# Kernel tuning notes

Measured on AMD Instinct MI355X. Metric: run time of the kernel, lower is better.

Reference implementation:

```python
import jax, jax.numpy as jnp
import numpy as np

ATTN_DIM = 1024
LATENT_DIM = 1024
N_HEADS = 16
HEAD_SIZE = ATTN_DIM // N_HEADS


def setup_inputs() -> dict:
    key = jax.random.key(0)
    ks = jax.random.split(key, 7)
    B, T = 2, 2048
    s_in = 1.0 / np.sqrt(LATENT_DIM)
    s_a = 1.0 / np.sqrt(ATTN_DIM)
    return {
        "x": jax.random.normal(ks[0], (B, T, LATENT_DIM), jnp.float32),
        "w_attn": jax.random.normal(ks[1], (LATENT_DIM, ATTN_DIM), jnp.float32) * s_in,
        "b_attn": jnp.zeros((ATTN_DIM,), jnp.float32),
        "w_qkv": jax.random.normal(ks[2], (ATTN_DIM, 3 * ATTN_DIM), jnp.float32) * s_a,
        "b_qkv": jnp.zeros((3 * ATTN_DIM,), jnp.float32),
        "w_proj": jax.random.normal(ks[3], (ATTN_DIM, ATTN_DIM), jnp.float32) * s_a,
        "b_proj": jnp.zeros((ATTN_DIM,), jnp.float32),
    }


def reference(x, w_attn, b_attn, w_qkv, b_qkv, w_proj, b_proj):
    # x: [B, T, latent_dim]
    h = jnp.einsum("btl,lc->btc", x, w_attn) + b_attn  # [B,T,C]
    B, T, C = h.shape
    qkv = jnp.einsum("btc,cd->btd", h, w_qkv) + b_qkv  # [B,T,3C]
    q, k, v = jnp.split(qkv, 3, axis=2)
    def heads(t):  # [B,T,C] -> [B,H,T,hs]
        return t.reshape(B, T, N_HEADS, HEAD_SIZE).transpose(0, 2, 1, 3)
    q, k, v = heads(q), heads(k), heads(v)
    scale = 1.0 / np.sqrt(HEAD_SIZE)
    scores = jnp.einsum("bhqd,bhkd->bhqk", q, k) * scale  # [B,H,T,T]
    attn = jax.nn.softmax(scores, axis=-1)
    out = jnp.einsum("bhqk,bhkd->bhqd", attn, v)  # [B,H,T,hs]
    out = out.transpose(0, 2, 1, 3).reshape(B, T, C)
    return jnp.einsum("btc,cd->btd", out, w_proj) + b_proj
```

## Files before the change

kernel.cpp:

```cpp
#include <hip/hip_runtime.h>

typedef unsigned short u16;
typedef unsigned int u32;
typedef __bf16 bf16x8 __attribute__((ext_vector_type(8)));
typedef float f32x4 __attribute__((ext_vector_type(4)));
typedef float f32x16 __attribute__((ext_vector_type(16)));
typedef unsigned uint2v __attribute__((ext_vector_type(2)));

typedef const __attribute__((address_space(1))) void* gcp_t;
typedef __attribute__((address_space(3))) void* lp_t;
#define GLDS16(g, l) __builtin_amdgcn_global_load_lds((gcp_t)(g), (lp_t)(l), 16, 0, 0)

__device__ __forceinline__ u16 f2bf(float f) {
  unsigned int u = __builtin_bit_cast(unsigned int, f);
  u += 0x7fffu + ((u >> 16) & 1u);
  return (u16)(u >> 16);
}
__device__ __forceinline__ u16 bfc(float f) {
  return __builtin_bit_cast(u16, (__bf16)f);
}
__device__ __forceinline__ u32 pkbf(float lo, float hi) {
  return (u32)bfc(lo) | ((u32)bfc(hi) << 16);
}
__device__ __forceinline__ float ex2(float x) {
  return __builtin_amdgcn_exp2f(x);
}

__global__ __launch_bounds__(256) void prep(const float* __restrict__ x, u16* __restrict__ xb,
                                            const float* __restrict__ wa, u16* __restrict__ wTa,
                                            const float* __restrict__ wq, u16* __restrict__ wTq,
                                            const float* __restrict__ wp, u16* __restrict__ wTp) {
  __shared__ float tile[32][33];
  const int idx = (int)blockIdx.x;
  const int tid = (int)threadIdx.x;
  if (idx < 2048) {
    long i = ((long)idx * 256 + tid) * 8;
    float4 a = *(const float4*)(x + i);
    float4 b = *(const float4*)(x + i + 4);
    union { u16 u[8]; int4 v; } pk;
    pk.u[0] = f2bf(a.x); pk.u[1] = f2bf(a.y); pk.u[2] = f2bf(a.z); pk.u[3] = f2bf(a.w);
    pk.u[4] = f2bf(b.x); pk.u[5] = f2bf(b.y); pk.u[6] = f2bf(b.z); pk.u[7] = f2bf(b.w);
    *(int4*)(xb + i) = pk.v;
    return;
  }
  const float* in; u16* out; int K, N, bx, by;
  if (idx < 3072) {
    int id = idx - 2048; in = wa; out = wTa; K = 1024; N = 1024; bx = id & 31; by = id >> 5;
  } else if (idx < 6144) {
    int id = idx - 3072; in = wq; out = wTq; K = 1024; N = 3072; bx = id % 96; by = id / 96;
  } else {
    int id = idx - 6144; in = wp; out = wTp; K = 1024; N = 1024; bx = id & 31; by = id >> 5;
  }
  const int n0 = bx * 32, k0 = by * 32;
  const int tx = tid & 31, ty = tid >> 5;
#pragma unroll
  for (int i = 0; i < 4; ++i)
    tile[ty + i * 8][tx] = in[(long)(k0 + ty + i * 8) * N + n0 + tx];
  __syncthreads();
#pragma unroll
  for (int i = 0; i < 4; ++i)
    out[(long)(n0 + ty + i * 8) * K + k0 + tx] = f2bf(tile[tx][ty + i * 8]);
}

template <int BM, int BN, int WN_WAVES, typename OutT, bool VSPLIT = false>
__global__ __launch_bounds__(256) void gemm_bt(const u16* __restrict__ A,
                                               const u16* __restrict__ Bt,
                                               const float* __restrict__ bias,
                                               OutT* __restrict__ C,
                                               u16* __restrict__ vout,
                                               int M, int N, int K) {
  constexpr int WM = BM / (4 / WN_WAVES);
  constexpr int WN = BN / WN_WAVES;
  constexpr int MF = WM / 16, NF = WN / 16;
  constexpr int STG = 2 * BM * 32 + 2 * BN * 32;
  constexpr int TRN = VSPLIT ? 128 * 136 : 0;
  constexpr int PSZ = STG > TRN ? STG : TRN;
  __shared__ __align__(16) u16 pool[PSZ];
  u16* lA0 = pool;
  u16* lB0 = pool + 2 * BM * 32;
  const int tid = (int)threadIdx.x;
  const int ln = tid & 63;
  const int w = tid >> 6;
  const int wr = w / WN_WAVES, wc = w % WN_WAVES;
  const int lr = ln & 15, lg = ln >> 4;

  const int nwg = (int)(gridDim.x * gridDim.y);
  const int lin = (int)(blockIdx.y * gridDim.x + blockIdx.x);
  const int cpx = nwg >> 3;
  const int swzb = (lin & 7) * cpx + (lin >> 3);
  const int bx = swzb % (int)gridDim.x;
  const int by = swzb / (int)gridDim.x;
  const long mBase = (long)by * BM;
  const long nBase = (long)bx * BN;

  f32x4 acc[MF][NF] = {};

  const int r0 = ln >> 2;
  const int c0 = (ln & 3) * 8;

  auto stage = [&](int buf, int k0) {
#pragma unroll
    for (int i = 0; i < BM / 64; ++i) {
      const int br = (i * 4 + w) * 16;
      GLDS16(A + (mBase + br + r0) * K + k0 + c0, lA0 + buf * BM * 32 + br * 32);
    }
#pragma unroll
    for (int i = 0; i < BN / 64; ++i) {
      const int br = (i * 4 + w) * 16;
      GLDS16(Bt + (nBase + br + r0) * K + k0 + c0, lB0 + buf * BN * 32 + br * 32);
    }
  };

  stage(0, 0);
  __syncthreads();
  int cur = 0;
  for (int k0 = 0; k0 < K; k0 += 32) {
    if (k0 + 32 < K) stage(cur ^ 1, k0 + 32);
    bf16x8 af[MF], bfv[NF];
#pragma unroll
    for (int mi = 0; mi < MF; ++mi)
      af[mi] = *(const bf16x8*)&lA0[cur * BM * 32 + (wr * WM + mi * 16 + lr) * 32 + lg * 8];
#pragma unroll
    for (int ni = 0; ni < NF; ++ni)
      bfv[ni] = *(const bf16x8*)&lB0[cur * BN * 32 + (wc * WN + ni * 16 + lr) * 32 + lg * 8];
#pragma unroll
    for (int mi = 0; mi < MF; ++mi)
#pragma unroll
      for (int ni = 0; ni < NF; ++ni)
        acc[mi][ni] = __builtin_amdgcn_mfma_f32_16x16x32_bf16(af[mi], bfv[ni],
                                                              acc[mi][ni], 0, 0, 0);
    __syncthreads();
    cur ^= 1;
  }

  if (VSPLIT && nBase >= 2048) {
#pragma unroll
    for (int ni = 0; ni < NF; ++ni) {
      const int cl = wc * WN + ni * 16 + lr;
      const float bv = bias[nBase + cl];
#pragma unroll
      for (int mi = 0; mi < MF; ++mi) {
#pragma unroll
        for (int j = 0; j < 4; ++j) {
          const int rl = wr * WM + mi * 16 + lg * 4 + j;
          pool[cl * 136 + rl] = bfc(acc[mi][ni][j] + bv);
        }
      }
    }
    __syncthreads();
    const int c = tid >> 1, half = tid & 1;
    const long cglob = nBase + c - 2048;
    const int hh2 = (int)(cglob >> 6), d = (int)(cglob & 63);
    const int bb = (int)(mBase >> 11);
    const int t0 = (int)(mBase & 2047);
    u16* dst = vout + ((long)(bb * 16 + hh2) * 64 + d) * 2048 + t0 + half * 64;
    const u16* srcp = &pool[c * 136 + half * 64];
#pragma unroll
    for (int i = 0; i < 8; ++i)
      *(int4*)(dst + i * 8) = *(const int4*)(srcp + i * 8);
    return;
  }

#pragma unroll
  for (int ni = 0; ni < NF; ++ni) {
    const long col = nBase + wc * WN + ni * 16 + lr;
    const float bv = bias[col];
#pragma unroll
    for (int mi = 0; mi < MF; ++mi) {
      const long row = mBase + wr * WM + mi * 16 + lg * 4;
#pragma unroll
      for (int j = 0; j < 4; ++j) {
        float v = acc[mi][ni][j] + bv;
        if constexpr (sizeof(OutT) == 2) {
          C[(row + j) * N + col] = (OutT)f2bf(v);
        } else {
          C[(row + j) * N + col] = v;
        }
      }
    }
  }
}

__global__ __launch_bounds__(512, 4) void attn_fwd(const u16* __restrict__ qkv,
                                                   const u16* __restrict__ vt,
                                                   u16* __restrict__ outp) {
  __shared__ __align__(16) u16 smemf[32768];
  const int tid = (int)threadIdx.x;
  const int ln = tid & 63;
  const int l31 = tid & 31;
  const int hiH = (tid >> 5) & 1;
  const int w = tid >> 6;
  const int g = w >> 2;
  const int qw = w & 3;
  const int bid0 = (int)blockIdx.x;
  const int bid = ((bid0 & 7) << 6) | (bid0 >> 3);
  const int qt = bid & 15;
  const int bh = bid >> 4;
  const int b = bh >> 4;
  const int hh = bh & 15;

  const float SCALE = 0.125f * 1.44269504088896f;

  const long qrow = (long)(b * 2048 + qt * 128 + qw * 32 + l31);
  const u16* Qp = qkv + qrow * 3072 + hh * 64;
  bf16x8 qf[4];
#pragma unroll
  for (int ks = 0; ks < 4; ++ks) {
    union { u16 u[8]; int4 i4; bf16x8 v; } in, ov;
    in.i4 = *(const int4*)(Qp + ks * 16 + hiH * 8);
#pragma unroll
    for (int e = 0; e < 8; ++e) {
      float f = __builtin_bit_cast(float, (u32)in.u[e] << 16) * SCALE;
      ov.u[e] = f2bf(f);
    }
    qf[ks] = ov.v;
  }

  f32x16 o[2] = {};
  float mrow = -1e30f, lsum = 0.f;

  const u16* Kbase = qkv + ((long)b * 2048) * 3072 + 1024 + hh * 64;
  const u16* Vbase = vt + (long)bh * 64 * 2048;

  const int sr = ln >> 3;
  const int scm = ln & 7;

  const int sw = (l31 & 7) << 4;
  const char* lds0 = (const char*)smemf + g * 32768 + l31 * 128;
  const char* kbse[4];
#pragma unroll
  for (int ks = 0; ks < 4; ++ks) kbse[ks] = lds0 + ((ks * 32 + hiH * 16) ^ sw);

  auto stageKV = [&](int buf, int t) {
    const int kv0 = (g * 16 + t) * 64;
    u16* dstK = smemf + g * 16384 + buf * 8192;
#pragma unroll
    for (int i = 0; i < 2; ++i) {
      const int br = (i * 4 + qw) * 8;
      const int r = br + sr;
      const int cs = scm ^ (r & 7);
      GLDS16(Kbase + (long)(kv0 + r) * 3072 + cs * 8, dstK + br * 64);
      GLDS16(Vbase + (long)r * 2048 + kv0 + cs * 8, dstK + 4096 + br * 64);
    }
  };

  stageKV(0, 0);
  __syncthreads();

  auto tile = [&](int buf, int kt) {
    if (kt + 1 < 16) stageKV(buf ^ 1, kt + 1);
    const int boff = buf * 16384;

    f32x16 st[2] = {};
#pragma unroll
    for (int t = 0; t < 2; ++t)
#pragma unroll
      for (int ks = 0; ks < 4; ++ks) {
        const bf16x8 kf = *(const bf16x8*)(kbse[ks] + boff + t * 4096);
        st[t] = __builtin_amdgcn_mfma_f32_32x32x16_bf16(kf, qf[ks], st[t], 0, 0, 0);
      }

    float mv[32];
#pragma unroll
    for (int t = 0; t < 2; ++t)
#pragma unroll
      for (int r = 0; r < 16; ++r) mv[t * 16 + r] = st[t][r];
    float m1[11];
#pragma unroll
    for (int i = 0; i < 10; ++i)
      m1[i] = fmaxf(fmaxf(mv[3 * i], mv[3 * i + 1]), mv[3 * i + 2]);
    m1[10] = fmaxf(mv[30], mv[31]);
    float m2[4];
    m2[0] = fmaxf(fmaxf(m1[0], m1[1]), m1[2]);
    m2[1] = fmaxf(fmaxf(m1[3], m1[4]), m1[5]);
    m2[2] = fmaxf(fmaxf(m1[6], m1[7]), m1[8]);
    m2[3] = fmaxf(m1[9], m1[10]);
    float mx = fmaxf(fmaxf(fmaxf(m2[0], m2[1]), m2[2]), m2[3]);
    mx = fmaxf(mx, __shfl_xor(mx, 32));

    if (!__all(mx <= mrow + 8.0f)) {
      const float mnew = fmaxf(mrow, mx);
      const float sf = ex2(mrow - mnew);
      mrow = mnew;
      lsum *= sf;
      o[0] *= sf;
      o[1] *= sf;
    }

#pragma unroll
    for (int t = 0; t < 2; ++t)
#pragma unroll
      for (int r = 0; r < 16; ++r) st[t][r] = ex2(st[t][r] - mrow);

    float ts[16];
#pragma unroll
    for (int r = 0; r < 16; ++r) ts[r] = st[0][r] + st[1][r];
#pragma unroll
    for (int s = 8; s > 0; s >>= 1)
#pragma unroll
      for (int r = 0; r < 8; ++r)
        if (r < s) ts[r] += ts[r + s];
    lsum += ts[0];

    bf16x8 pa[4];
#pragma unroll
    for (int t = 0; t < 2; ++t)
#pragma unroll
      for (int gg = 0; gg < 2; ++gg) {
        const int bse = gg * 8;
        u32 A = pkbf(st[t][bse + 0], st[t][bse + 1]);
        u32 B = pkbf(st[t][bse + 2], st[t][bse + 3]);
        u32 C = pkbf(st[t][bse + 4], st[t][bse + 5]);
        u32 D = pkbf(st[t][bse + 6], st[t][bse + 7]);
        union { u32 wv[4]; bf16x8 v; } u;
#if __has_builtin(__builtin_amdgcn_permlane32_swap)
        uint2v r0 = __builtin_amdgcn_permlane32_swap(A, C, false, false);
        uint2v r1 = __builtin_amdgcn_permlane32_swap(B, D, false, false);
        u.wv[0] = r0[0]; u.wv[1] = r1[0]; u.wv[2] = r0[1]; u.wv[3] = r1[1];
#else
        const u32 sA = __shfl_xor((int)A, 32);
        const u32 sB = __shfl_xor((int)B, 32);
        const u32 sC = __shfl_xor((int)C, 32);
        const u32 sD = __shfl_xor((int)D, 32);
        u.wv[0] = hiH ? sC : A;
        u.wv[1] = hiH ? sD : B;
        u.wv[2] = hiH ? C : sA;
        u.wv[3] = hiH ? D : sB;
#endif
        pa[t * 2 + gg] = u.v;
      }

#pragma unroll
    for (int dt = 0; dt < 2; ++dt)
#pragma unroll
      for (int ks2 = 0; ks2 < 4; ++ks2) {
        const bf16x8 vf = *(const bf16x8*)(kbse[ks2] + boff + 8192 + dt * 4096);
        o[dt] = __builtin_amdgcn_mfma_f32_32x32x16_bf16(vf, pa[ks2], o[dt], 0, 0, 0);
      }
    __syncthreads();
  };

  for (int k8 = 0; k8 < 8; ++k8) {
    tile(0, k8 * 2);
    tile(1, k8 * 2 + 1);
  }

  const float lsum_tot = lsum + __shfl_xor(lsum, 32);
  float* PO = (float*)smemf;
  float* MLf = (float*)((char*)smemf + 32768);

  if (g == 1) {
    float* dst = PO + (w - 4) * 2048 + ln * 32;
#pragma unroll
    for (int dt = 0; dt < 2; ++dt)
#pragma unroll
      for (int q4 = 0; q4 < 4; ++q4) {
        f32x4 c;
#pragma unroll
        for (int j = 0; j < 4; ++j) c[j] = o[dt][q4 * 4 + j];
        *(f32x4*)(dst + dt * 16 + q4 * 4) = c;
      }
    MLf[(w - 4) * 128 + ln * 2] = mrow;
    MLf[(w - 4) * 128 + ln * 2 + 1] = lsum_tot;
  }
  __syncthreads();
  if (g == 0) {
    const float m1v = MLf[w * 128 + ln * 2];
    const float l1 = MLf[w * 128 + ln * 2 + 1];
    const float* src = PO + w * 2048 + ln * 32;
    const float m = fmaxf(mrow, m1v);
    const float a0 = ex2(mrow - m);
    const float a1 = ex2(m1v - m);
    const float linv = 1.0f / (lsum_tot * a0 + l1 * a1);
    u16* T = (u16*)((char*)smemf + 36864) + w * (32 * 72);
#pragma unroll
    for (int dt = 0; dt < 2; ++dt) {
      float o1[16];
#pragma unroll
      for (int q4 = 0; q4 < 4; ++q4) {
        const f32x4 c = *(const f32x4*)(src + dt * 16 + q4 * 4);
#pragma unroll
        for (int j = 0; j < 4; ++j) o1[q4 * 4 + j] = c[j];
      }
#pragma unroll
      for (int r = 0; r < 16; ++r) {
        const float v = (o[dt][r] * a0 + o1[r] * a1) * linv;
        const int d = (r & 3) + 8 * (r >> 2) + 4 * hiH + dt * 32;
        T[l31 * 72 + d] = bfc(v);
      }
    }
    asm volatile("s_waitcnt lgkmcnt(0)" ::: "memory");
    __builtin_amdgcn_sched_barrier(0);
    const int rr = ln >> 1;
    const int c0 = (ln & 1) * 32;
    u16* orow = outp + ((long)(b * 2048 + qt * 128 + w * 32 + rr)) * 1024 + hh * 64 + c0;
#pragma unroll
    for (int i = 0; i < 4; ++i)
      *(int4*)(orow + i * 8) = *(const int4*)&T[rr * 72 + c0 + i * 8];
  }
}

extern "C" void kernel_launch(void* const* d_in, const int* in_sizes, int n_in,
                              void* d_out, int out_size, void* d_ws, size_t ws_size,
                              hipStream_t stream) {
  (void)in_sizes; (void)n_in; (void)out_size;
  const float* x = (const float*)d_in[0];
  const float* b_attn = (const float*)d_in[2];
  const float* b_qkv = (const float*)d_in[4];
  const float* b_proj = (const float*)d_in[6];

  char* ws = (char*)d_ws;
  const size_t MB = 1024 * 1024;
  u16* xb   = (u16*)(ws + 0 * MB);
  u16* hbuf = (u16*)(ws + 8 * MB);
  u16* qkvb = (u16*)(ws + 16 * MB);
  u16* vtb  = (u16*)(ws + 40 * MB);
  u16* aout = (u16*)(ws + 48 * MB);
  u16* wTa  = (u16*)(ws + 56 * MB);
  u16* wTq  = (u16*)(ws + 58 * MB);
  u16* wTp  = (u16*)(ws + 64 * MB);
  if (ws_size < 66 * MB) return;

  prep<<<7168, 256, 0, stream>>>(x, xb, (const float*)d_in[1], wTa,
                                 (const float*)d_in[3], wTq,
                                 (const float*)d_in[5], wTp);

  gemm_bt<64, 128, 4, u16><<<dim3(8, 64), 256, 0, stream>>>(
      xb, wTa, b_attn, hbuf, nullptr, 4096, 1024, 1024);
  gemm_bt<128, 128, 2, u16, true><<<dim3(24, 32), 256, 0, stream>>>(
      hbuf, wTq, b_qkv, qkvb, vtb, 4096, 3072, 1024);
  attn_fwd<<<512, 512, 0, stream>>>(qkvb, vtb, aout);
  gemm_bt<64, 128, 4, float><<<dim3(8, 64), 256, 0, stream>>>(
      aout, wTp, b_proj, (float*)d_out, nullptr, 4096, 1024, 1024);
}
```

Baseline: 151.3 us.

## Software-pipeline attention loop with 32-wide KV tiles and four-stage LDS ring

Restructures the flash-attention inner loop into 32-key tiles held in a four-buffer LDS ring. Loads are issued three tiles ahead, and the QK MFMA for the next tile runs before the softmax of the current one. Row-sum accumulation is split across eight partial accumulators to shorten dependency chains. The aim is to overlap MFMA work with the softmax VALU work and to hide global-to-LDS latency. The cost is twice as many barriers per key, since tiles are smaller, plus more register pressure from the extra score tile.

```diff
diff --git a/kernel.cpp b/kernel.cpp
--- a/kernel.cpp
+++ b/kernel.cpp
@@ -200,6 +200,7 @@
   const int hh = bh & 15;
 
   const float SCALE = 0.125f * 1.44269504088896f;
+  const f32x16 fzero = {};
 
   const long qrow = (long)(b * 2048 + qt * 128 + qw * 32 + l31);
   const u16* Qp = qkv + qrow * 3072 + hh * 64;
@@ -217,135 +218,128 @@
   }
 
   f32x16 o[2] = {};
-  float mrow = -1e30f, lsum = 0.f;
+  float ls8[8] = {};
+  float mrow = -1e30f;
 
   const u16* Kbase = qkv + ((long)b * 2048) * 3072 + 1024 + hh * 64;
   const u16* Vbase = vt + (long)bh * 64 * 2048;
 
-  const int sr = ln >> 3;
-  const int scm = ln & 7;
-
-  const int sw = (l31 & 7) << 4;
-  const char* lds0 = (const char*)smemf + g * 32768 + l31 * 128;
-  const char* kbse[4];
-#pragma unroll
-  for (int ks = 0; ks < 4; ++ks) kbse[ks] = lds0 + ((ks * 32 + hiH * 16) ^ sw);
-
-  auto stageKV = [&](int buf, int t) {
-    const int kv0 = (g * 16 + t) * 64;
-    u16* dstK = smemf + g * 16384 + buf * 8192;
-#pragma unroll
-    for (int i = 0; i < 2; ++i) {
-      const int br = (i * 4 + qw) * 8;
-      const int r = br + sr;
-      const int cs = scm ^ (r & 7);
-      GLDS16(Kbase + (long)(kv0 + r) * 3072 + cs * 8, dstK + br * 64);
-      GLDS16(Vbase + (long)r * 2048 + kv0 + cs * 8, dstK + 4096 + br * 64);
-    }
+  const char* kchar = (const char*)smemf + g * 32768 + l31 * 128;
+  const char* vchar = (const char*)smemf + g * 32768 + 4096 + l31 * 64;
+  const char* kptr[4];
+  const char* vptr[2];
+#pragma unroll
+  for (int ks = 0; ks < 4; ++ks)
+    kptr[ks] = kchar + ((ks * 32 + hiH * 16) ^ ((l31 & 7) << 4));
+#pragma unroll
+  for (int ks = 0; ks < 2; ++ks)
+    vptr[ks] = vchar + ((ks * 32 + hiH * 16) ^ ((l31 & 3) << 4));
+
+  auto stageKV = [&](int bf, int t) {
+    const int kv0 = g * 1024 + t * 32;
+    u16* dst = smemf + g * 16384 + bf * 4096;
+    const int rk = qw * 8 + (ln >> 3);
+    const int csk = (ln & 7) ^ (rk & 7);
+    GLDS16(Kbase + (long)(kv0 + rk) * 3072 + csk * 8, dst + qw * 512);
+    const int rv = qw * 16 + (ln >> 2);
+    const int csv = (ln & 3) ^ (rv & 3);
+    GLDS16(Vbase + (long)rv * 2048 + kv0 + csv * 8, dst + 2048 + qw * 512);
   };
 
-  stageKV(0, 0);
-  __syncthreads();
-
-  auto tile = [&](int buf, int kt) {
-    if (kt + 1 < 16) stageKV(buf ^ 1, kt + 1);
-    const int boff = buf * 16384;
-
-    f32x16 st[2] = {};
-#pragma unroll
-    for (int t = 0; t < 2; ++t)
-#pragma unroll
-      for (int ks = 0; ks < 4; ++ks) {
-        const bf16x8 kf = *(const bf16x8*)(kbse[ks] + boff + t * 4096);
-        st[t] = __builtin_amdgcn_mfma_f32_32x32x16_bf16(kf, qf[ks], st[t], 0, 0, 0);
-      }
-
-    float mv[32];
-#pragma unroll
-    for (int t = 0; t < 2; ++t)
-#pragma unroll
-      for (int r = 0; r < 16; ++r) mv[t * 16 + r] = st[t][r];
-    float m1[11];
-#pragma unroll
-    for (int i = 0; i < 10; ++i)
-      m1[i] = fmaxf(fmaxf(mv[3 * i], mv[3 * i + 1]), mv[3 * i + 2]);
-    m1[10] = fmaxf(mv[30], mv[31]);
-    float m2[4];
-    m2[0] = fmaxf(fmaxf(m1[0], m1[1]), m1[2]);
-    m2[1] = fmaxf(fmaxf(m1[3], m1[4]), m1[5]);
-    m2[2] = fmaxf(fmaxf(m1[6], m1[7]), m1[8]);
-    m2[3] = fmaxf(m1[9], m1[10]);
-    float mx = fmaxf(fmaxf(fmaxf(m2[0], m2[1]), m2[2]), m2[3]);
+  auto qk = [&](int bf, f32x16& stN) {
+    stN = fzero;
+#pragma unroll
+    for (int ks = 0; ks < 4; ++ks) {
+      const bf16x8 kf = *(const bf16x8*)(kptr[ks] + bf * 8192);
+      stN = __builtin_amdgcn_mfma_f32_32x32x16_bf16(kf, qf[ks], stN, 0, 0, 0);
+    }
+  };
+
+  auto body = [&](int t, int bN, int bC, int bS, f32x16& stC, f32x16& stN) {
+    if (t + 1 < 32) qk(bN, stN);
+
+    float a0 = fmaxf(fmaxf(stC[0], stC[1]), stC[2]);
+    float a1 = fmaxf(fmaxf(stC[3], stC[4]), stC[5]);
+    float a2 = fmaxf(fmaxf(stC[6], stC[7]), stC[8]);
+    float a3 = fmaxf(fmaxf(stC[9], stC[10]), stC[11]);
+    float a4 = fmaxf(fmaxf(stC[12], stC[13]), stC[14]);
+    float b0 = fmaxf(fmaxf(a0, a1), a2);
+    float b1 = fmaxf(fmaxf(a3, a4), stC[15]);
+    float mx = fmaxf(b0, b1);
     mx = fmaxf(mx, __shfl_xor(mx, 32));
 
     if (!__all(mx <= mrow + 8.0f)) {
       const float mnew = fmaxf(mrow, mx);
       const float sf = ex2(mrow - mnew);
       mrow = mnew;
-      lsum *= sf;
+#pragma unroll
+      for (int r = 0; r < 8; ++r) ls8[r] *= sf;
       o[0] *= sf;
       o[1] *= sf;
     }
-
-#pragma unroll
-    for (int t = 0; t < 2; ++t)
-#pragma unroll
-      for (int r = 0; r < 16; ++r) st[t][r] = ex2(st[t][r] - mrow);
-
-    float ts[16];
-#pragma unroll
-    for (int r = 0; r < 16; ++r) ts[r] = st[0][r] + st[1][r];
-#pragma unroll
-    for (int s = 8; s > 0; s >>= 1)
-#pragma unroll
-      for (int r = 0; r < 8; ++r)
-        if (r < s) ts[r] += ts[r + s];
-    lsum += ts[0];
-
-    bf16x8 pa[4];
-#pragma unroll
-    for (int t = 0; t < 2; ++t)
-#pragma unroll
-      for (int gg = 0; gg < 2; ++gg) {
-        const int bse = gg * 8;
-        u32 A = pkbf(st[t][bse + 0], st[t][bse + 1]);
-        u32 B = pkbf(st[t][bse + 2], st[t][bse + 3]);
-        u32 C = pkbf(st[t][bse + 4], st[t][bse + 5]);
-        u32 D = pkbf(st[t][bse + 6], st[t][bse + 7]);
-        union { u32 wv[4]; bf16x8 v; } u;
+#pragma unroll
+    for (int r = 0; r < 16; ++r) stC[r] = ex2(stC[r] - mrow);
+#pragma unroll
+    for (int r = 0; r < 8; ++r) ls8[r] += stC[r] + stC[r + 8];
+
+    bf16x8 pa[2];
+#pragma unroll
+    for (int gg = 0; gg < 2; ++gg) {
+      const int bse = gg * 8;
+      u32 A = pkbf(stC[bse + 0], stC[bse + 1]);
+      u32 B = pkbf(stC[bse + 2], stC[bse + 3]);
+      u32 C = pkbf(stC[bse + 4], stC[bse + 5]);
+      u32 D = pkbf(stC[bse + 6], stC[bse + 7]);
+      union { u32 wv[4]; bf16x8 v; } u;
 #if __has_builtin(__builtin_amdgcn_permlane32_swap)
-        uint2v r0 = __builtin_amdgcn_permlane32_swap(A, C, false, false);
-        uint2v r1 = __builtin_amdgcn_permlane32_swap(B, D, false, false);
-        u.wv[0] = r0[0]; u.wv[1] = r1[0]; u.wv[2] = r0[1]; u.wv[3] = r1[1];
+      uint2v r0 = __builtin_amdgcn_permlane32_swap(A, C, false, false);
+      uint2v r1 = __builtin_amdgcn_permlane32_swap(B, D, false, false);
+      u.wv[0] = r0[0]; u.wv[1] = r1[0]; u.wv[2] = r0[1]; u.wv[3] = r1[1];
 #else
-        const u32 sA = __shfl_xor((int)A, 32);
-        const u32 sB = __shfl_xor((int)B, 32);
-        const u32 sC = __shfl_xor((int)C, 32);
-        const u32 sD = __shfl_xor((int)D, 32);
-        u.wv[0] = hiH ? sC : A;
-        u.wv[1] = hiH ? sD : B;
-        u.wv[2] = hiH ? C : sA;
-        u.wv[3] = hiH ? D : sB;
+      const u32 sA = __shfl_xor((int)A, 32);
+      const u32 sB = __shfl_xor((int)B, 32);
+      const u32 sC = __shfl_xor((int)C, 32);
+      const u32 sD = __shfl_xor((int)D, 32);
+      u.wv[0] = hiH ? sC : A;
+      u.wv[1] = hiH ? sD : B;
+      u.wv[2] = hiH ? C : sA;
+      u.wv[3] = hiH ? D : sB;
 #endif
-        pa[t * 2 + gg] = u.v;
-      }
-
+      pa[gg] = u.v;
+    }
 #pragma unroll
     for (int dt = 0; dt < 2; ++dt)
 #pragma unroll
-      for (int ks2 = 0; ks2 < 4; ++ks2) {
-        const bf16x8 vf = *(const bf16x8*)(kbse[ks2] + boff + 8192 + dt * 4096);
+      for (int ks2 = 0; ks2 < 2; ++ks2) {
+        const bf16x8 vf = *(const bf16x8*)(vptr[ks2] + bC * 8192 + dt * 2048);
         o[dt] = __builtin_amdgcn_mfma_f32_32x32x16_bf16(vf, pa[ks2], o[dt], 0, 0, 0);
       }
+
     __syncthreads();
+    if (t + 3 < 32) stageKV(bS, t + 3);
   };
 
-  for (int k8 = 0; k8 < 8; ++k8) {
-    tile(0, k8 * 2);
-    tile(1, k8 * 2 + 1);
-  }
-
+  f32x16 stA, stB;
+  stageKV(0, 0);
+  __syncthreads();
+  stageKV(1, 1);
+  qk(0, stA);
+  __syncthreads();
+  stageKV(2, 2);
+
+  for (int tb = 0; tb < 32; tb += 4) {
+    body(tb + 0, 1, 0, 3, stA, stB);
+    body(tb + 1, 2, 1, 0, stB, stA);
+    body(tb + 2, 3, 2, 1, stA, stB);
+    body(tb + 3, 0, 3, 2, stB, stA);
+  }
+
+  float t4[4];
+#pragma unroll
+  for (int r = 0; r < 4; ++r) t4[r] = ls8[r] + ls8[r + 4];
+  float lsum = (t4[0] + t4[1]) + (t4[2] + t4[3]);
   const float lsum_tot = lsum + __shfl_xor(lsum, 32);
+
   float* PO = (float*)smemf;
   float* MLf = (float*)((char*)smemf + 32768);
 
```

Result: no change. 151.3 us (-0.0%).
